# Kernel tuning notes

Hardware: AMD Instinct MI355X
Metric: run time of the kernel (lower is better)

The kernel has to match this reference:

```python
import jax, jax.numpy as jnp
import numpy as np

N_LAYERS, N_QUBITS = 2, 2
BATCH = 2_097_152

# CNOT matrices in the kron(wire0, wire1) basis (wire0 = most significant bit)
_CNOT01 = jnp.array([[1,0,0,0],[0,1,0,0],[0,0,0,1],[0,0,1,0]], dtype=jnp.complex64)  # control 0 -> target 1
_CNOT10 = jnp.array([[1,0,0,0],[0,0,0,1],[0,0,1,0],[0,1,0,0]], dtype=jnp.complex64)  # control 1 -> target 0


def _rot(phi, theta, omega):
    # PennyLane Rot(phi, theta, omega) = RZ(omega) @ RY(theta) @ RZ(phi)
    c, s = jnp.cos(theta * 0.5), jnp.sin(theta * 0.5)
    ep = jnp.exp(-0.5j * (phi + omega))   # e^{-i(phi+omega)/2}
    em = jnp.exp(0.5j * (phi - omega))    # e^{ i(phi-omega)/2}
    return jnp.stack([
        jnp.stack([ep * c, -em * s]),
        jnp.stack([jnp.conj(em) * s, jnp.conj(ep) * c]),
    ])


def _circuit_unitary(params):
    # StronglyEntanglingLayers on 2 wires: per layer Rot on each wire, then
    # CNOT(0->1) and CNOT(1->0) (range r=1, periodic boundary).
    U = jnp.eye(4, dtype=jnp.complex64)
    for l in range(N_LAYERS):
        r0 = _rot(params[l, 0, 0], params[l, 0, 1], params[l, 0, 2])
        r1 = _rot(params[l, 1, 0], params[l, 1, 1], params[l, 1, 2])
        U = _CNOT10 @ (_CNOT01 @ (jnp.kron(r0, r1) @ U))
    return U


def setup_inputs() -> dict:
    key = jax.random.key(0)
    k1, k2, k3, k4 = jax.random.split(key, 4)
    return {
        "x": jax.random.normal(k1, (BATCH, N_QUBITS), dtype=jnp.float32),
        "q_params": 0.01 * jax.random.normal(k2, (N_LAYERS, N_QUBITS, 3), dtype=jnp.float32),
        "fc_w": jax.random.normal(k3, (1, 1), dtype=jnp.float32),
        "fc_b": jax.random.normal(k4, (1,), dtype=jnp.float32),
    }


def reference(x, q_params, fc_w, fc_b):
    # AngleEmbedding (RY) on |00>: state = kron(RY(x0)|0>, RY(x1)|0>)
    half = 0.5 * x
    c, s = jnp.cos(half), jnp.sin(half)                 # [B, 2]
    psi0 = jnp.stack([c[:, 0] * c[:, 1],
                      c[:, 0] * s[:, 1],
                      s[:, 0] * c[:, 1],
                      s[:, 0] * s[:, 1]], axis=-1).astype(jnp.complex64)  # [B, 4]
    U = _circuit_unitary(q_params)                      # [4, 4] complex64, batch-shared
    psi = psi0 @ U.T                                    # [B, 4] final state
    p = jnp.real(psi) ** 2 + jnp.imag(psi) ** 2          # probabilities
    ev = p[:, 0] + p[:, 1] - p[:, 2] - p[:, 3]           # <Z on wire 0>
    return ev[:, None] @ fc_w.T + fc_b                   # Linear(1,1) -> [B, 1]
```

## Files before the change

### kernel.cpp

```cpp
#include <hip/hip_runtime.h>


struct C2 { float re, im; };
__device__ inline C2 cmul(C2 a, C2 b) { return {a.re*b.re - a.im*b.im, a.re*b.im + a.im*b.re}; }
__device__ inline C2 cadd(C2 a, C2 b) { return {a.re + b.re, a.im + b.im}; }

__device__ inline void qnn_build_form(const float* __restrict__ qp,
                                      const float* __restrict__ fc_w,
                                      const float* __restrict__ fc_b,
                                      float* __restrict__ A, float* __restrict__ bout) {
    C2 U[4][4];
#pragma unroll
    for (int i = 0; i < 4; i++)
#pragma unroll
        for (int j = 0; j < 4; j++)
            U[i][j] = { (i == j) ? 1.f : 0.f, 0.f };

#pragma unroll
    for (int l = 0; l < 2; l++) {
        C2 r[2][2][2];
#pragma unroll
        for (int w = 0; w < 2; w++) {
            float phi = qp[(l*2 + w)*3 + 0];
            float th  = qp[(l*2 + w)*3 + 1];
            float om  = qp[(l*2 + w)*3 + 2];
            float c, s, epre, epim, emre, emim;
            __sincosf(0.5f * th, &s, &c);
            __sincosf(-0.5f * (phi + om), &epim, &epre);
            __sincosf( 0.5f * (phi - om), &emim, &emre);
            r[w][0][0] = {  epre * c,  epim * c };
            r[w][0][1] = { -emre * s, -emim * s };
            r[w][1][0] = {  emre * s, -emim * s };
            r[w][1][1] = {  epre * c, -epim * c };
        }
        C2 Un[4][4];
#pragma unroll
        for (int a = 0; a < 2; a++)
#pragma unroll
            for (int b = 0; b < 2; b++) {
                int i = 2*a + b;
#pragma unroll
                for (int j = 0; j < 4; j++) {
                    C2 acc = {0.f, 0.f};
#pragma unroll
                    for (int c = 0; c < 2; c++)
#pragma unroll
                        for (int d = 0; d < 2; d++) {
                            int k = 2*c + d;
                            C2 kij = cmul(r[0][a][c], r[1][b][d]);
                            acc = cadd(acc, cmul(kij, U[k][j]));
                        }
                    Un[i][j] = acc;
                }
            }
#pragma unroll
        for (int j = 0; j < 4; j++) { C2 t = Un[2][j]; Un[2][j] = Un[3][j]; Un[3][j] = t; }
#pragma unroll
        for (int j = 0; j < 4; j++) { C2 t = Un[1][j]; Un[1][j] = Un[3][j]; Un[3][j] = t; }
#pragma unroll
        for (int i = 0; i < 4; i++)
#pragma unroll
            for (int j = 0; j < 4; j++)
                U[i][j] = Un[i][j];
    }

    float w0 = fc_w[0];
#pragma unroll
    for (int i = 0; i < 4; i++)
#pragma unroll
        for (int j = 0; j < 4; j++) {
            float acc = 0.f;
#pragma unroll
            for (int k = 0; k < 4; k++) {
                float d = (k < 2) ? 1.f : -1.f;
                acc += d * (U[k][i].re * U[k][j].re + U[k][i].im * U[k][j].im);
            }
            A[i*4 + j] = w0 * acc;
        }
    *bout = fc_b[0];
}

__global__ __launch_bounds__(256) void qnn_fused_kernel(
        const float4* __restrict__ x,
        const float* __restrict__ qp,
        const float* __restrict__ fc_w,
        const float* __restrict__ fc_b,
        float4* __restrict__ out,
        int n4) {
    float A[16], b;
    qnn_build_form(qp, fc_w, fc_b, A, &b);

    int stride = gridDim.x * blockDim.x;
    for (int t = blockIdx.x * blockDim.x + threadIdx.x; t < n4; t += stride) {
        float4 xa = x[2*t];
        float4 xb = x[2*t + 1];
        float xs[8] = { xa.x, xa.y, xa.z, xa.w, xb.x, xb.y, xb.z, xb.w };

        float oo[4];
#pragma unroll
        for (int e = 0; e < 4; e++) {
            float s0, c0, s1, c1;
            __sincosf(0.5f * xs[2*e],     &s0, &c0);
            __sincosf(0.5f * xs[2*e + 1], &s1, &c1);
            float v0 = c0*c1, v1 = c0*s1, v2 = s0*c1, v3 = s0*s1;
            float ev = v0*(A[0]*v0  + A[1]*v1  + A[2]*v2  + A[3]*v3)
                     + v1*(A[4]*v0  + A[5]*v1  + A[6]*v2  + A[7]*v3)
                     + v2*(A[8]*v0  + A[9]*v1  + A[10]*v2 + A[11]*v3)
                     + v3*(A[12]*v0 + A[13]*v1 + A[14]*v2 + A[15]*v3);
            oo[e] = ev + b;
        }
        out[t] = make_float4(oo[0], oo[1], oo[2], oo[3]);
    }
}

extern "C" void kernel_launch(void* const* d_in, const int* in_sizes, int n_in,
                              void* d_out, int out_size, void* d_ws, size_t ws_size,
                              hipStream_t stream) {
    const float* x    = (const float*)d_in[0];
    const float* qp   = (const float*)d_in[1];
    const float* fc_w = (const float*)d_in[2];
    const float* fc_b = (const float*)d_in[3];
    float* out = (float*)d_out;

    int n  = in_sizes[0] / 2;
    int n4 = n / 4;

    int block = 256;
    int grid  = 1024;
    qnn_fused_kernel<<<grid, block, 0, stream>>>(
        (const float4*)x, qp, fc_w, fc_b, (float4*)out, n4);
}
```

Measured before the change: 76.06 us.

## Collapse quadratic form to a 9-coefficient trig expansion and hoist setup into its own kernel

Double-angle identities rewrite the 4x4 quadratic form in half-angle products as a 9-term bilinear expression in cos/sin of the full angles. That removes the half-angle scaling and most of the per-element multiplies. The circuit-unitary build moves to a one-thread setup kernel that writes the coefficients to workspace, so every streaming thread no longer recomputes it. The grid becomes size-dependent, capped at 2048 blocks. The cost is an extra kernel launch and a dependency on the workspace being available; without it the code falls back to the fused kernel.

```diff
diff --git a/kernel.cpp b/kernel.cpp
--- a/kernel.cpp
+++ b/kernel.cpp
@@ -5,10 +5,10 @@
 __device__ inline C2 cmul(C2 a, C2 b) { return {a.re*b.re - a.im*b.im, a.re*b.im + a.im*b.re}; }
 __device__ inline C2 cadd(C2 a, C2 b) { return {a.re + b.re, a.im + b.im}; }
 
-__device__ inline void qnn_build_form(const float* __restrict__ qp,
-                                      const float* __restrict__ fc_w,
-                                      const float* __restrict__ fc_b,
-                                      float* __restrict__ A, float* __restrict__ bout) {
+__device__ inline void qnn_build_K(const float* __restrict__ qp,
+                                   const float* __restrict__ fc_w,
+                                   const float* __restrict__ fc_b,
+                                   float* __restrict__ K) {
     C2 U[4][4];
 #pragma unroll
     for (int i = 0; i < 4; i++)
@@ -65,6 +65,7 @@
     }
 
     float w0 = fc_w[0];
+    float A[16];
 #pragma unroll
     for (int i = 0; i < 4; i++)
 #pragma unroll
@@ -77,7 +78,71 @@
             }
             A[i*4 + j] = w0 * acc;
         }
-    *bout = fc_b[0];
+
+    float A00 = A[0],  A11 = A[5],  A22 = A[10], A33 = A[15];
+    float a01 = A[1] + A[4];
+    float a23 = A[11] + A[14];
+    float a02 = A[2] + A[8];
+    float a13 = A[7] + A[13];
+    float a03 = A[3] + A[12];
+    float a12 = A[6] + A[9];
+
+    K[0] = 0.25f * (A00 + A11 + A22 + A33) + fc_b[0];
+    K[1] = 0.25f * (A00 + A11 - A22 - A33);
+    K[2] = 0.25f * (a02 + a13);
+    K[3] = 0.25f * (A00 - A11 + A22 - A33);
+    K[4] = 0.25f * (A00 - A11 - A22 + A33);
+    K[5] = 0.25f * (a02 - a13);
+    K[6] = 0.25f * (a01 + a23);
+    K[7] = 0.25f * (a01 - a23);
+    K[8] = 0.25f * (a03 + a12);
+}
+
+__global__ void qnn_setup_kernel(const float* __restrict__ qp,
+                                 const float* __restrict__ fc_w,
+                                 const float* __restrict__ fc_b,
+                                 float* __restrict__ Kout) {
+    float K[9];
+    qnn_build_K(qp, fc_w, fc_b, K);
+    if (threadIdx.x == 0) {
+#pragma unroll
+        for (int i = 0; i < 9; i++) Kout[i] = K[i];
+    }
+}
+
+__device__ inline float qnn_eval(float x0, float x1,
+                                 float K0, float K1, float K2,
+                                 float K3, float K4, float K5,
+                                 float K6, float K7, float K8) {
+    float s0, c0, s1, c1;
+    __sincosf(x0, &s0, &c0);
+    __sincosf(x1, &s1, &c1);
+    float e0 = fmaf(K2, s0, fmaf(K1, c0, K0));
+    float e1 = fmaf(K5, s0, fmaf(K4, c0, K3));
+    float e2 = fmaf(K8, s0, fmaf(K7, c0, K6));
+    return fmaf(s1, e2, fmaf(c1, e1, e0));
+}
+
+__global__ __launch_bounds__(256) void qnn_stream_kernel(
+        const float4* __restrict__ x,
+        const float* __restrict__ Kin,
+        float4* __restrict__ out,
+        int n4) {
+    float K0 = Kin[0], K1 = Kin[1], K2 = Kin[2];
+    float K3 = Kin[3], K4 = Kin[4], K5 = Kin[5];
+    float K6 = Kin[6], K7 = Kin[7], K8 = Kin[8];
+
+    int stride = gridDim.x * blockDim.x;
+    for (int t = blockIdx.x * blockDim.x + threadIdx.x; t < n4; t += stride) {
+        float4 xa = x[2*t];
+        float4 xb = x[2*t + 1];
+        float4 o;
+        o.x = qnn_eval(xa.x, xa.y, K0,K1,K2,K3,K4,K5,K6,K7,K8);
+        o.y = qnn_eval(xa.z, xa.w, K0,K1,K2,K3,K4,K5,K6,K7,K8);
+        o.z = qnn_eval(xb.x, xb.y, K0,K1,K2,K3,K4,K5,K6,K7,K8);
+        o.w = qnn_eval(xb.z, xb.w, K0,K1,K2,K3,K4,K5,K6,K7,K8);
+        out[t] = o;
+    }
 }
 
 __global__ __launch_bounds__(256) void qnn_fused_kernel(
@@ -87,29 +152,18 @@
         const float* __restrict__ fc_b,
         float4* __restrict__ out,
         int n4) {
-    float A[16], b;
-    qnn_build_form(qp, fc_w, fc_b, A, &b);
-
+    float K[9];
+    qnn_build_K(qp, fc_w, fc_b, K);
     int stride = gridDim.x * blockDim.x;
     for (int t = blockIdx.x * blockDim.x + threadIdx.x; t < n4; t += stride) {
         float4 xa = x[2*t];
         float4 xb = x[2*t + 1];
-        float xs[8] = { xa.x, xa.y, xa.z, xa.w, xb.x, xb.y, xb.z, xb.w };
-
-        float oo[4];
-#pragma unroll
-        for (int e = 0; e < 4; e++) {
-            float s0, c0, s1, c1;
-            __sincosf(0.5f * xs[2*e],     &s0, &c0);
-            __sincosf(0.5f * xs[2*e + 1], &s1, &c1);
-            float v0 = c0*c1, v1 = c0*s1, v2 = s0*c1, v3 = s0*s1;
-            float ev = v0*(A[0]*v0  + A[1]*v1  + A[2]*v2  + A[3]*v3)
-                     + v1*(A[4]*v0  + A[5]*v1  + A[6]*v2  + A[7]*v3)
-                     + v2*(A[8]*v0  + A[9]*v1  + A[10]*v2 + A[11]*v3)
-                     + v3*(A[12]*v0 + A[13]*v1 + A[14]*v2 + A[15]*v3);
-            oo[e] = ev + b;
-        }
-        out[t] = make_float4(oo[0], oo[1], oo[2], oo[3]);
+        float4 o;
+        o.x = qnn_eval(xa.x, xa.y, K[0],K[1],K[2],K[3],K[4],K[5],K[6],K[7],K[8]);
+        o.y = qnn_eval(xa.z, xa.w, K[0],K[1],K[2],K[3],K[4],K[5],K[6],K[7],K[8]);
+        o.z = qnn_eval(xb.x, xb.y, K[0],K[1],K[2],K[3],K[4],K[5],K[6],K[7],K[8]);
+        o.w = qnn_eval(xb.z, xb.w, K[0],K[1],K[2],K[3],K[4],K[5],K[6],K[7],K[8]);
+        out[t] = o;
     }
 }
 
@@ -126,7 +180,16 @@
     int n4 = n / 4;
 
     int block = 256;
-    int grid  = 1024;
-    qnn_fused_kernel<<<grid, block, 0, stream>>>(
-        (const float4*)x, qp, fc_w, fc_b, (float4*)out, n4);
+    int grid  = (n4 + block - 1) / block;
+    if (grid > 2048) grid = 2048;
+
+    if (ws_size >= 64 && d_ws != nullptr) {
+        float* Kws = (float*)d_ws;
+        qnn_setup_kernel<<<1, 64, 0, stream>>>(qp, fc_w, fc_b, Kws);
+        qnn_stream_kernel<<<grid, block, 0, stream>>>(
+            (const float4*)x, Kws, (float4*)out, n4);
+    } else {
+        qnn_fused_kernel<<<grid, block, 0, stream>>>(
+            (const float4*)x, qp, fc_w, fc_b, (float4*)out, n4);
+    }
 }
```

New measurement: 82.16 us. +8.0%, slower.
